# Performance work log

Measured on AMD Instinct MI355X. Metric: run time of the kernel, lower is better.

Reference implementation:

```python
import jax, jax.numpy as jnp
import numpy as np

D = 1024
H = 16
HD = D // H
B = 2
T = 2048


def _rope_tables(t, hd):
    inv_freq = 1.0 / (10000.0 ** (np.arange(0, hd, 2, dtype=np.float32) / hd))
    ang = np.arange(t, dtype=np.float32)[:, None] * inv_freq[None, :]  # [T, hd/2]
    emb = np.concatenate([ang, ang], axis=-1)  # [T, hd]
    return jnp.asarray(np.cos(emb)), jnp.asarray(np.sin(emb))


def setup_inputs() -> dict:
    key = jax.random.key(0)
    kx, kq, kk, kv, ko = jax.random.split(key, 5)
    scale = 0.02
    x = jax.random.normal(kx, (B, T, D), dtype=jnp.float32)
    cos, sin = _rope_tables(T, HD)
    mask = jnp.tril(jnp.ones((T, T), dtype=jnp.int32))[None, None]  # [1,1,T,T]
    wq = jax.random.normal(kq, (D, D), dtype=jnp.float32) * scale
    wk = jax.random.normal(kk, (D, D), dtype=jnp.float32) * scale
    wv = jax.random.normal(kv, (D, D), dtype=jnp.float32) * scale
    wo = jax.random.normal(ko, (D, D), dtype=jnp.float32) * scale
    return {"x": x, "cos": cos, "sin": sin, "mask": mask,
            "wq": wq, "wk": wk, "wv": wv, "wo": wo}


def _rotate_half(t):
    t1, t2 = jnp.split(t, 2, axis=-1)
    return jnp.concatenate((-t2, t1), axis=-1)


def reference(x, cos, sin, mask, wq, wk, wv, wo):
    Bx, Tx, C = x.shape
    hd = C // H
    # nn.Linear: y = x @ W.T  -> [B,T,H,hd] -> [B,H,T,hd]
    q = (x @ wq.T).reshape(Bx, Tx, H, hd).transpose(0, 2, 1, 3)
    k = (x @ wk.T).reshape(Bx, Tx, H, hd).transpose(0, 2, 1, 3)
    v = (x @ wv.T).reshape(Bx, Tx, H, hd).transpose(0, 2, 1, 3)
    c = cos[:Tx][None, None]  # [1,1,T,hd]
    s = sin[:Tx][None, None]
    q = q * c + _rotate_half(q) * s
    k = k * c + _rotate_half(k) * s
    att = jnp.einsum('bhqd,bhkd->bhqk', q, k) * (hd ** -0.5)
    att = jnp.where(mask[:, :, :Tx, :Tx] == 0, -jnp.inf, att)
    att = jax.nn.softmax(att, axis=-1)
    out = jnp.einsum('bhqk,bhkd->bhqd', att, v)
    out = out.transpose(0, 2, 1, 3).reshape(Bx, Tx, C)
    return out @ wo.T
```

## Files before the change

### kernel.cpp

```cpp
#include <hip/hip_runtime.h>
#include <math.h>

constexpr int D  = 1024;
constexpr int H  = 16;
constexpr int HD = 64;
constexpr int B  = 2;
constexpr int T  = 2048;
constexpr int M  = B * T;

constexpr size_t XSZ = (size_t)M * D;
constexpr size_t WSZ = (size_t)D * D;

typedef float  f32x4   __attribute__((ext_vector_type(4)));
typedef float  f32x16  __attribute__((ext_vector_type(16)));
typedef __bf16 bf16x8  __attribute__((ext_vector_type(8)));
typedef __bf16 bf16x4  __attribute__((ext_vector_type(4)));
typedef unsigned u32x2 __attribute__((ext_vector_type(2)));
typedef unsigned u32x4 __attribute__((ext_vector_type(4)));

static __device__ inline f32x4 mfma16(bf16x8 a, bf16x8 b, f32x4 c) {
  return __builtin_amdgcn_mfma_f32_16x16x32_bf16(a, b, c, 0, 0, 0);
}
static __device__ inline f32x16 mfma32(bf16x8 a, bf16x8 b, f32x16 c) {
  return __builtin_amdgcn_mfma_f32_32x32x16_bf16(a, b, c, 0, 0, 0);
}
static __device__ inline unsigned cvtpk(float a, float b) {
  unsigned r;
  asm("v_cvt_pk_bf16_f32 %0, %1, %2" : "=v"(r) : "v"(a), "v"(b));
  return r;
}
static __device__ inline u32x2 plswap(unsigned a, unsigned b) {
  return __builtin_amdgcn_permlane32_swap(a, b, false, false);
}
static __device__ inline void gload16(const __bf16* g, __bf16* l) {
  __builtin_amdgcn_global_load_lds(
      (const __attribute__((address_space(1))) void*)g,
      (__attribute__((address_space(3))) void*)l, 16, 0, 0);
}

__global__ __launch_bounds__(256)
void cvt_all(const float* __restrict__ x, const float* __restrict__ wq,
             const float* __restrict__ wk, const float* __restrict__ wv,
             const float* __restrict__ wo, __bf16* __restrict__ out) {
  size_t idx = ((size_t)blockIdx.x * 256 + threadIdx.x) * 8;
  const float* src;
  if      (idx < XSZ)            src = x  + idx;
  else if (idx < XSZ + WSZ)      src = wq + (idx - XSZ);
  else if (idx < XSZ + 2 * WSZ)  src = wk + (idx - XSZ - WSZ);
  else if (idx < XSZ + 3 * WSZ)  src = wv + (idx - XSZ - 2 * WSZ);
  else                           src = wo + (idx - XSZ - 3 * WSZ);
  float4 a = *reinterpret_cast<const float4*>(src);
  float4 b = *reinterpret_cast<const float4*>(src + 4);
  bf16x8 o;
  o[0] = (__bf16)a.x; o[1] = (__bf16)a.y; o[2] = (__bf16)a.z; o[3] = (__bf16)a.w;
  o[4] = (__bf16)b.x; o[5] = (__bf16)b.y; o[6] = (__bf16)b.z; o[7] = (__bf16)b.w;
  *reinterpret_cast<bf16x8*>(out + idx) = o;
}

template<int MODE>
__global__ __launch_bounds__(256)
void gemm_mfma(const __bf16* __restrict__ A,
               const __bf16* __restrict__ W0, const __bf16* __restrict__ W1,
               const __bf16* __restrict__ W2,
               const float* __restrict__ cosT, const float* __restrict__ sinT,
               void* __restrict__ out0, void* __restrict__ out1,
               void* __restrict__ out2) {
  constexpr int BM  = (MODE == 0) ? 64 : 128;
  constexpr int NMT = BM / 32;
  __shared__ __bf16 As[BM * 64];
  __shared__ __bf16 Bs[128 * 64];

  const int tid  = threadIdx.x;
  const int lane = tid & 63;
  const int w    = tid >> 6;
  const int wm   = w >> 1;
  const int wn   = w & 1;
  const int l15  = lane & 15, lg = lane >> 4;
  const int m0   = blockIdx.y * BM;

  int which, n0;
  const __bf16* Bw;
  if (MODE == 1) {
    which = blockIdx.x >> 3;
    n0 = (blockIdx.x & 7) * 128;
    Bw = which == 0 ? W0 : which == 1 ? W1 : W2;
  } else {
    which = 0;
    n0 = blockIdx.x * 128;
    Bw = W0;
  }

  f32x4 acc[NMT][4];
  #pragma unroll
  for (int i = 0; i < NMT; ++i)
    #pragma unroll
    for (int j = 0; j < 4; ++j) acc[i][j] = (f32x4){0.f, 0.f, 0.f, 0.f};

  const int r0 = tid >> 3;
  const int c0 = (tid & 7) * 8;

  for (int k0 = 0; k0 < 1024; k0 += 64) {
    #pragma unroll
    for (int i = 0; i < BM / 32; ++i)
      gload16(A + (size_t)(m0 + r0 + 32 * i) * 1024 + k0 + c0,
              As + (tid + 256 * i) * 8);
    #pragma unroll
    for (int i = 0; i < 4; ++i)
      gload16(Bw + (size_t)(n0 + r0 + 32 * i) * 1024 + k0 + c0,
              Bs + (tid + 256 * i) * 8);
    __syncthreads();

    #pragma unroll
    for (int ks = 0; ks < 2; ++ks) {
      bf16x8 af[NMT], bfr[4];
      #pragma unroll
      for (int mt = 0; mt < NMT; ++mt)
        af[mt] = *reinterpret_cast<const bf16x8*>(
            &As[(wm * (BM / 2) + mt * 16 + l15) * 64 + ks * 32 + lg * 8]);
      #pragma unroll
      for (int nt = 0; nt < 4; ++nt)
        bfr[nt] = *reinterpret_cast<const bf16x8*>(
            &Bs[(wn * 64 + nt * 16 + l15) * 64 + ks * 32 + lg * 8]);
      #pragma unroll
      for (int mt = 0; mt < NMT; ++mt)
        #pragma unroll
        for (int nt = 0; nt < 4; ++nt)
          acc[mt][nt] = mfma16(af[mt], bfr[nt], acc[mt][nt]);
    }
    __syncthreads();
  }

  if (MODE == 0) {
    float* o = (float*)out0;
    #pragma unroll
    for (int mt = 0; mt < NMT; ++mt) {
      const int mb = m0 + wm * (BM / 2) + mt * 16 + lg * 4;
      #pragma unroll
      for (int nt = 0; nt < 4; ++nt) {
        const int n = n0 + wn * 64 + nt * 16 + l15;
        #pragma unroll
        for (int r = 0; r < 4; ++r)
          o[(size_t)(mb + r) * 1024 + n] = acc[mt][nt][r];
      }
    }
  } else if (which < 2) {
    __bf16* dst = which == 0 ? (__bf16*)out0 : (__bf16*)out1;
    const float qs = (which == 0) ? 0.180336880f : 1.0f;
    const int h = (n0 + wn * 64) >> 6;
    const int e  = l15 & 7;
    const int Lh = (l15 >> 3) << 5;
    #pragma unroll
    for (int mt = 0; mt < NMT; ++mt) {
      const int tb   = m0 + wm * (BM / 2) + mt * 16 + lg * 4;
      const int bb   = tb >> 11;
      const int tloc = tb & 2047;
      const int bh   = bb * H + h;
      #pragma unroll
      for (int r = 0; r < 4; ++r) {
        const int t = tloc + r;
        const int L = (t & 31) + Lh;
        size_t fb;
        if (which == 0)
          fb = ((size_t)bh * 64 + (t >> 5)) * 4;
        else
          fb = (((size_t)bh * 32 + (t >> 6)) * 2 + ((t >> 5) & 1)) * 4;
        #pragma unroll
        for (int nt = 0; nt < 2; ++nt) {
          const int hd = nt * 16 + l15;
          const float c = cosT[t * HD + hd];
          const float s = sinT[t * HD + hd];
          const float v1 = acc[mt][nt][r];
          const float v2 = acc[mt][nt + 2][r];
          dst[(fb + nt)     * 512 + L * 8 + e] = (__bf16)((v1 * c - v2 * s) * qs);
          dst[(fb + nt + 2) * 512 + L * 8 + e] = (__bf16)((v2 * c + v1 * s) * qs);
        }
      }
    }
  } else {
    __bf16* dst = (__bf16*)out2;
    const int h = (n0 + wn * 64) >> 6;
    #pragma unroll
    for (int mt = 0; mt < NMT; ++mt) {
      const int tb   = m0 + wm * (BM / 2) + mt * 16 + lg * 4;
      const int bb   = tb >> 11;
      const int tloc = tb & 2047;
      const int bh   = bb * H + h;
      const int jt   = tloc >> 6;
      const int kt   = tloc & 63;
      const int Lk   = ((kt >> 3) & 1) << 5;
      const int e0   = kt & 7;
      const size_t fb = (((size_t)bh * 32 + jt) * 2) * 4 + (kt >> 4);
      #pragma unroll
      for (int nt = 0; nt < 4; ++nt) {
        const int hd = nt * 16 + l15;
        const int dg = hd >> 5;
        const int L  = (hd & 31) + Lk;
        bf16x4 ov;
        #pragma unroll
        for (int r = 0; r < 4; ++r) ov[r] = (__bf16)acc[mt][nt][r];
        *reinterpret_cast<bf16x4*>(
            &dst[(fb + (size_t)dg * 4) * 512 + L * 8 + e0]) = ov;
      }
    }
  }
}

__global__ __launch_bounds__(256, 2)
void attn_v15(const __bf16* __restrict__ Qf, const __bf16* __restrict__ Kf,
              const __bf16* __restrict__ Vf, __bf16* __restrict__ Ob) {
  const int tid  = threadIdx.x;
  const int lane = tid & 63;
  const int w    = tid >> 6;
  const int l31  = lane & 31;
  const int hi   = lane >> 5;
  const int bx   = blockIdx.x;
  const int by   = blockIdx.y;
  const int bh   = (bx & 7) + 8 * (by >> 3);
  const int x    = (bx >> 3) + 2 * (by & 7);

  const int wi = (bh < 16) ? w : (w ^ 1);
  const int qt = (wi == 0) ? 2 * x : (wi == 1) ? 63 - 2 * x
               : (wi == 2) ? 2 * x + 1 : 62 - 2 * x;
  const int q0w = qt * 32;
  const int NT  = (qt >> 1) + 1;

  const __bf16* qbase = Qf + (((size_t)bh * 64 + qt) * 4) * 512 + lane * 8;
  bf16x8 qfr[4];
  #pragma unroll
  for (int st = 0; st < 4; ++st)
    qfr[st] = *reinterpret_cast<const bf16x8*>(qbase + st * 512);

  f32x16 zv;
  #pragma unroll
  for (int i = 0; i < 16; ++i) zv[i] = 0.f;

  float m_run = -INFINITY, l_run = 0.f;
  f32x16 oacc0, oacc1;
  #pragma unroll
  for (int i = 0; i < 16; ++i) { oacc0[i] = 0.f; oacc1[i] = 0.f; }

  const __bf16* kbase = Kf + ((size_t)bh * 32 * 8) * 512 + lane * 8;
  const __bf16* vbase = Vf + ((size_t)bh * 32 * 8) * 512 + lane * 8;

#define LOADK8(K0, K1, K2, K3, K4, K5, K6, K7, jj)                            \
  do {                                                                        \
    const __bf16* _kp = kbase + (size_t)(jj) * 8 * 512;                       \
    K0 = *reinterpret_cast<const bf16x8*>(_kp);                               \
    K1 = *reinterpret_cast<const bf16x8*>(_kp + 512);                         \
    K2 = *reinterpret_cast<const bf16x8*>(_kp + 1024);                        \
    K3 = *reinterpret_cast<const bf16x8*>(_kp + 1536);                        \
    K4 = *reinterpret_cast<const bf16x8*>(_kp + 2048);                        \
    K5 = *reinterpret_cast<const bf16x8*>(_kp + 2560);                        \
    K6 = *reinterpret_cast<const bf16x8*>(_kp + 3072);                        \
    K7 = *reinterpret_cast<const bf16x8*>(_kp + 3584);                        \
    __builtin_amdgcn_sched_barrier(0);                                        \
  } while (0)

#define LOADV8(jj)                                                            \
  do {                                                                        \
    const __bf16* _vp = vbase + (size_t)(jj) * 8 * 512;                       \
    VV0 = *reinterpret_cast<const bf16x8*>(_vp);                              \
    VV1 = *reinterpret_cast<const bf16x8*>(_vp + 512);                        \
    VV2 = *reinterpret_cast<const bf16x8*>(_vp + 1024);                       \
    VV3 = *reinterpret_cast<const bf16x8*>(_vp + 1536);                       \
    VV4 = *reinterpret_cast<const bf16x8*>(_vp + 2048);                       \
    VV5 = *reinterpret_cast<const bf16x8*>(_vp + 2560);                       \
    VV6 = *reinterpret_cast<const bf16x8*>(_vp + 3072);                       \
    VV7 = *reinterpret_cast<const bf16x8*>(_vp + 3584);                       \
    __builtin_amdgcn_sched_barrier(0);                                        \
  } while (0)

#define QK64(SV0, SV1, K0, K1, K2, K3, K4, K5, K6, K7)                        \
  do {                                                                        \
    SV0 = mfma32(K0, qfr[0], zv);                                             \
    SV0 = mfma32(K1, qfr[1], SV0);                                            \
    SV0 = mfma32(K2, qfr[2], SV0);                                            \
    SV0 = mfma32(K3, qfr[3], SV0);                                            \
    SV1 = mfma32(K4, qfr[0], zv);                                             \
    SV1 = mfma32(K5, qfr[1], SV1);                                            \
    SV1 = mfma32(K6, qfr[2], SV1);                                            \
    SV1 = mfma32(K7, qfr[3], SV1);                                            \
  } while (0)

#define SMPV(SV0, SV1, jj)                                                    \
  do {                                                                        \
    if ((jj) == NT - 1) {         \
      const int _q  = q0w + l31;                                              \
      const int _k0 = (jj) * 64 + 4 * hi;                                     \
      _Pragma("unroll")                                                       \
      for (int _r = 0; _r < 16; ++_r) {                                       \
        const int _key = _k0 + (_r & 3) + 8 * (_r >> 2);                      \
        if (_key > _q)      SV0[_r] = -INFINITY;                              \
        if (_key + 32 > _q) SV1[_r] = -INFINITY;                              \
      }                                                                       \
    }                                                                         \
    float _mx[16];                                                            \
    _Pragma("unroll")                                                         \
    for (int _i = 0; _i < 16; ++_i) _mx[_i] = fmaxf(SV0[_i], SV1[_i]);        \
    _Pragma("unroll")                                                         \
    for (int _s = 8; _s > 0; _s >>= 1)                                        \
      _Pragma("unroll")                                                       \
      for (int _i = 0; _i < 8; ++_i)                                          \
        if (_i < _s) _mx[_i] = fmaxf(_mx[_i], _mx[_i + _s]);                  \
    union { float f; unsigned u; } _cv; _cv.f = _mx[0];                       \
    u32x2 _sw = plswap(_cv.u, _cv.u);                                         \
    union { unsigned u; float f; } _c0, _c1; _c0.u = _sw[0]; _c1.u = _sw[1];  \
    const float _pmax = fmaxf(_c0.f, _c1.f);                                  \
    if (__any(_pmax > m_run + 8.f)) {                                         \
      const float _mn = fmaxf(m_run, _pmax);                                  \
      const float _rs = exp2f(m_run - _mn);                                   \
      l_run *= _rs;                                                           \
      _Pragma("unroll")                                                       \
      for (int _i = 0; _i < 16; ++_i) { oacc0[_i] *= _rs; oacc1[_i] *= _rs; } \
      m_run = _mn;                                                            \
    }                                                                         \
    _Pragma("unroll")                                                         \
    for (int _i = 0; _i < 16; ++_i) {                                         \
      SV0[_i] = exp2f(SV0[_i] - m_run);                                       \
      SV1[_i] = exp2f(SV1[_i] - m_run);                                       \
    }                                                                         \
    float _sm[16];                                                            \
    _Pragma("unroll")                                                         \
    for (int _i = 0; _i < 16; ++_i) _sm[_i] = SV0[_i] + SV1[_i];              \
    _Pragma("unroll")                                                         \
    for (int _s = 8; _s > 0; _s >>= 1)                                        \
      _Pragma("unroll")                                                       \
      for (int _i = 0; _i < 8; ++_i)                                          \
        if (_i < _s) _sm[_i] += _sm[_i + _s];                                 \
    l_run += _sm[0];                                                          \
    unsigned _cp0[8], _cp1[8];                                                \
    _Pragma("unroll")                                                         \
    for (int _m = 0; _m < 4; ++_m) {                                          \
      _cp0[2 * _m]     = cvtpk(SV0[4 * _m],     SV0[4 * _m + 1]);             \
      _cp0[2 * _m + 1] = cvtpk(SV0[4 * _m + 2], SV0[4 * _m + 3]);             \
      _cp1[2 * _m]     = cvtpk(SV1[4 * _m],     SV1[4 * _m + 1]);             \
      _cp1[2 * _m + 1] = cvtpk(SV1[4 * _m + 2], SV1[4 * _m + 3]);             \
    }                                                                         \
    {                                                                         \
      u32x2 _r0 = plswap(_cp0[0], _cp0[2]);                                   \
      u32x2 _r1 = plswap(_cp0[1], _cp0[3]);                                   \
      union { u32x4 u; bf16x8 v; } _pu;                                       \
      _pu.u = (u32x4){_r0[0], _r1[0], _r0[1], _r1[1]};                        \
      oacc0 = mfma32(VV0, _pu.v, oacc0);                                      \
      oacc1 = mfma32(VV4, _pu.v, oacc1);                                      \
    }                                                                         \
    {                                                                         \
      u32x2 _r0 = plswap(_cp0[4], _cp0[6]);                                   \
      u32x2 _r1 = plswap(_cp0[5], _cp0[7]);                                   \
      union { u32x4 u; bf16x8 v; } _pu;                                       \
      _pu.u = (u32x4){_r0[0], _r1[0], _r0[1], _r1[1]};                        \
      oacc0 = mfma32(VV1, _pu.v, oacc0);                                      \
      oacc1 = mfma32(VV5, _pu.v, oacc1);                                      \
    }                                                                         \
    {                                                                         \
      u32x2 _r0 = plswap(_cp1[0], _cp1[2]);                                   \
      u32x2 _r1 = plswap(_cp1[1], _cp1[3]);                                   \
      union { u32x4 u; bf16x8 v; } _pu;                                       \
      _pu.u = (u32x4){_r0[0], _r1[0], _r0[1], _r1[1]};                        \
      oacc0 = mfma32(VV2, _pu.v, oacc0);                                      \
      oacc1 = mfma32(VV6, _pu.v, oacc1);                                      \
    }                                                                         \
    {                                                                         \
      u32x2 _r0 = plswap(_cp1[4], _cp1[6]);                                   \
      u32x2 _r1 = plswap(_cp1[5], _cp1[7]);                                   \
      union { u32x4 u; bf16x8 v; } _pu;                                       \
      _pu.u = (u32x4){_r0[0], _r1[0], _r0[1], _r1[1]};                        \
      oacc0 = mfma32(VV3, _pu.v, oacc0);                                      \
      oacc1 = mfma32(VV7, _pu.v, oacc1);                                      \
    }                                                                         \
  } while (0)

  bf16x8 kA0, kA1, kA2, kA3, kA4, kA5, kA6, kA7;
  bf16x8 kB0, kB1, kB2, kB3, kB4, kB5, kB6, kB7;
  bf16x8 VV0, VV1, VV2, VV3, VV4, VV5, VV6, VV7;
  f32x16 svA0, svA1, svB0, svB1;

  LOADK8(kA0, kA1, kA2, kA3, kA4, kA5, kA6, kA7, 0);
  QK64(svA0, svA1, kA0, kA1, kA2, kA3, kA4, kA5, kA6, kA7);
  if (1 < NT) LOADK8(kB0, kB1, kB2, kB3, kB4, kB5, kB6, kB7, 1);

  int j = 0;
  #pragma unroll 1
  for (;;) {
    LOADV8(j);
    if (j + 1 < NT)
      QK64(svB0, svB1, kB0, kB1, kB2, kB3, kB4, kB5, kB6, kB7);
    if (j + 2 < NT)
      LOADK8(kA0, kA1, kA2, kA3, kA4, kA5, kA6, kA7, j + 2);
    SMPV(svA0, svA1, j);
    if (++j >= NT) break;

    LOADV8(j);
    if (j + 1 < NT)
      QK64(svA0, svA1, kA0, kA1, kA2, kA3, kA4, kA5, kA6, kA7);
    if (j + 2 < NT)
      LOADK8(kB0, kB1, kB2, kB3, kB4, kB5, kB6, kB7, j + 2);
    SMPV(svB0, svB1, j);
    if (++j >= NT) break;
  }
#undef SMPV
#undef QK64
#undef LOADV8
#undef LOADK8

  const float l_tot = l_run + __shfl_xor(l_run, 32);
  const float inv = 1.f / l_tot;
  const int b = bh >> 4, h = bh & 15;
  const int q_abs = q0w + l31;
  const size_t rowbase = ((size_t)(b * T + q_abs)) * 1024 + h * 64;
  #pragma unroll
  for (int rg = 0; rg < 4; ++rg) {
    bf16x4 o0, o1;
    #pragma unroll
    for (int r = 0; r < 4; ++r) {
      o0[r] = (__bf16)(oacc0[rg * 4 + r] * inv);
      o1[r] = (__bf16)(oacc1[rg * 4 + r] * inv);
    }
    *reinterpret_cast<bf16x4*>(&Ob[rowbase + rg * 8 + hi * 4])      = o0;
    *reinterpret_cast<bf16x4*>(&Ob[rowbase + 32 + rg * 8 + hi * 4]) = o1;
  }
}

extern "C" void kernel_launch(void* const* d_in, const int* in_sizes, int n_in,
                              void* d_out, int out_size, void* d_ws, size_t ws_size,
                              hipStream_t stream) {
  const float* x    = (const float*)d_in[0];
  const float* cosT = (const float*)d_in[1];
  const float* sinT = (const float*)d_in[2];
  const float* wq   = (const float*)d_in[4];
  const float* wk   = (const float*)d_in[5];
  const float* wv   = (const float*)d_in[6];
  const float* wo   = (const float*)d_in[7];
  float* out = (float*)d_out;

  __bf16* xb   = (__bf16*)d_ws;
  __bf16* wqb  = xb  + XSZ;
  __bf16* wkb  = wqb + WSZ;
  __bf16* wvb  = wkb + WSZ;
  __bf16* wob  = wvb + WSZ;
  __bf16* Qfb  = wob + WSZ;
  __bf16* Kfb  = Qfb + XSZ;
  __bf16* Vfb  = Kfb + XSZ;
  __bf16* attb = Vfb + XSZ;

  cvt_all<<<(XSZ + 4 * WSZ) / 8 / 256, 256, 0, stream>>>(x, wq, wk, wv, wo, xb);

  gemm_mfma<1><<<dim3(24, 32), 256, 0, stream>>>(
      xb, wqb, wkb, wvb, cosT, sinT, Qfb, Kfb, Vfb);

  attn_v15<<<dim3(16, 32), 256, 0, stream>>>(Qfb, Kfb, Vfb, attb);

  gemm_mfma<0><<<dim3(8, 64), 256, 0, stream>>>(
      attb, wob, nullptr, nullptr, nullptr, nullptr, out, nullptr, nullptr);
}
```

Before: 141.3 us.

## Share A tile across Q, K and V weights in fused QKV GEMM

The QKV projection kernel now has each block load one 64-row activation tile and all three weight tiles, computing the Q, K and V outputs together. Previously blocks were split by weight matrix with a 128-row A tile, so each activation tile was fetched three times. This trades A reuse for more shared memory (about 56KB) and three times the accumulator registers per thread, which may cut occupancy. The output projection is split into its own non-templated kernel with the same tiling as before.

```diff
diff --git a/kernel.cpp b/kernel.cpp
--- a/kernel.cpp
+++ b/kernel.cpp
@@ -57,18 +57,15 @@
   *reinterpret_cast<bf16x8*>(out + idx) = o;
 }
 
-template<int MODE>
 __global__ __launch_bounds__(256)
-void gemm_mfma(const __bf16* __restrict__ A,
-               const __bf16* __restrict__ W0, const __bf16* __restrict__ W1,
-               const __bf16* __restrict__ W2,
-               const float* __restrict__ cosT, const float* __restrict__ sinT,
-               void* __restrict__ out0, void* __restrict__ out1,
-               void* __restrict__ out2) {
-  constexpr int BM  = (MODE == 0) ? 64 : 128;
-  constexpr int NMT = BM / 32;
-  __shared__ __bf16 As[BM * 64];
-  __shared__ __bf16 Bs[128 * 64];
+void gemm_qkv(const __bf16* __restrict__ A,
+              const __bf16* __restrict__ W0, const __bf16* __restrict__ W1,
+              const __bf16* __restrict__ W2,
+              const float* __restrict__ cosT, const float* __restrict__ sinT,
+              __bf16* __restrict__ Qf, __bf16* __restrict__ Kf,
+              __bf16* __restrict__ Vf) {
+  __shared__ __bf16 As[64 * 64];
+  __shared__ __bf16 Bs[3][128 * 64];
 
   const int tid  = threadIdx.x;
   const int lane = tid & 63;
@@ -76,112 +73,98 @@
   const int wm   = w >> 1;
   const int wn   = w & 1;
   const int l15  = lane & 15, lg = lane >> 4;
-  const int m0   = blockIdx.y * BM;
-
-  int which, n0;
-  const __bf16* Bw;
-  if (MODE == 1) {
-    which = blockIdx.x >> 3;
-    n0 = (blockIdx.x & 7) * 128;
-    Bw = which == 0 ? W0 : which == 1 ? W1 : W2;
-  } else {
-    which = 0;
-    n0 = blockIdx.x * 128;
-    Bw = W0;
-  }
-
-  f32x4 acc[NMT][4];
-  #pragma unroll
-  for (int i = 0; i < NMT; ++i)
-    #pragma unroll
-    for (int j = 0; j < 4; ++j) acc[i][j] = (f32x4){0.f, 0.f, 0.f, 0.f};
+  const int m0   = blockIdx.y * 64;
+  const int n0   = blockIdx.x * 128;
+
+  f32x4 acc[3][2][4];
+  #pragma unroll
+  for (int ws = 0; ws < 3; ++ws)
+    #pragma unroll
+    for (int i = 0; i < 2; ++i)
+      #pragma unroll
+      for (int j = 0; j < 4; ++j) acc[ws][i][j] = (f32x4){0.f, 0.f, 0.f, 0.f};
 
   const int r0 = tid >> 3;
   const int c0 = (tid & 7) * 8;
 
   for (int k0 = 0; k0 < 1024; k0 += 64) {
-    #pragma unroll
-    for (int i = 0; i < BM / 32; ++i)
-      gload16(A + (size_t)(m0 + r0 + 32 * i) * 1024 + k0 + c0,
-              As + (tid + 256 * i) * 8);
-    #pragma unroll
-    for (int i = 0; i < 4; ++i)
-      gload16(Bw + (size_t)(n0 + r0 + 32 * i) * 1024 + k0 + c0,
-              Bs + (tid + 256 * i) * 8);
+    gload16(A + (size_t)(m0 + r0) * 1024 + k0 + c0,      As + tid * 8);
+    gload16(A + (size_t)(m0 + r0 + 32) * 1024 + k0 + c0, As + (tid + 256) * 8);
+    #pragma unroll
+    for (int i = 0; i < 4; ++i) {
+      const size_t go = (size_t)(n0 + r0 + 32 * i) * 1024 + k0 + c0;
+      gload16(W0 + go, Bs[0] + (tid + 256 * i) * 8);
+      gload16(W1 + go, Bs[1] + (tid + 256 * i) * 8);
+      gload16(W2 + go, Bs[2] + (tid + 256 * i) * 8);
+    }
     __syncthreads();
 
     #pragma unroll
     for (int ks = 0; ks < 2; ++ks) {
-      bf16x8 af[NMT], bfr[4];
-      #pragma unroll
-      for (int mt = 0; mt < NMT; ++mt)
+      bf16x8 af[2];
+      #pragma unroll
+      for (int mt = 0; mt < 2; ++mt)
         af[mt] = *reinterpret_cast<const bf16x8*>(
-            &As[(wm * (BM / 2) + mt * 16 + l15) * 64 + ks * 32 + lg * 8]);
-      #pragma unroll
-      for (int nt = 0; nt < 4; ++nt)
-        bfr[nt] = *reinterpret_cast<const bf16x8*>(
-            &Bs[(wn * 64 + nt * 16 + l15) * 64 + ks * 32 + lg * 8]);
-      #pragma unroll
-      for (int mt = 0; mt < NMT; ++mt)
+            &As[(wm * 32 + mt * 16 + l15) * 64 + ks * 32 + lg * 8]);
+      #pragma unroll
+      for (int ws = 0; ws < 3; ++ws) {
+        bf16x8 bfr[4];
         #pragma unroll
         for (int nt = 0; nt < 4; ++nt)
-          acc[mt][nt] = mfma16(af[mt], bfr[nt], acc[mt][nt]);
+          bfr[nt] = *reinterpret_cast<const bf16x8*>(
+              &Bs[ws][(wn * 64 + nt * 16 + l15) * 64 + ks * 32 + lg * 8]);
+        #pragma unroll
+        for (int mt = 0; mt < 2; ++mt)
+          #pragma unroll
+          for (int nt = 0; nt < 4; ++nt)
+            acc[ws][mt][nt] = mfma16(af[mt], bfr[nt], acc[ws][mt][nt]);
+      }
     }
     __syncthreads();
   }
 
-  if (MODE == 0) {
-    float* o = (float*)out0;
-    #pragma unroll
-    for (int mt = 0; mt < NMT; ++mt) {
-      const int mb = m0 + wm * (BM / 2) + mt * 16 + lg * 4;
-      #pragma unroll
-      for (int nt = 0; nt < 4; ++nt) {
-        const int n = n0 + wn * 64 + nt * 16 + l15;
-        #pragma unroll
-        for (int r = 0; r < 4; ++r)
-          o[(size_t)(mb + r) * 1024 + n] = acc[mt][nt][r];
-      }
-    }
-  } else if (which < 2) {
-    __bf16* dst = which == 0 ? (__bf16*)out0 : (__bf16*)out1;
-    const float qs = (which == 0) ? 0.180336880f : 1.0f;
-    const int h = (n0 + wn * 64) >> 6;
+  {
+    const int h  = (n0 + wn * 64) >> 6;
     const int e  = l15 & 7;
     const int Lh = (l15 >> 3) << 5;
     #pragma unroll
-    for (int mt = 0; mt < NMT; ++mt) {
-      const int tb   = m0 + wm * (BM / 2) + mt * 16 + lg * 4;
-      const int bb   = tb >> 11;
-      const int tloc = tb & 2047;
-      const int bh   = bb * H + h;
-      #pragma unroll
-      for (int r = 0; r < 4; ++r) {
-        const int t = tloc + r;
-        const int L = (t & 31) + Lh;
-        size_t fb;
-        if (which == 0)
-          fb = ((size_t)bh * 64 + (t >> 5)) * 4;
-        else
-          fb = (((size_t)bh * 32 + (t >> 6)) * 2 + ((t >> 5) & 1)) * 4;
+    for (int ws = 0; ws < 2; ++ws) {
+      __bf16* dst = (ws == 0) ? Qf : Kf;
+      const float qs = (ws == 0) ? 0.180336880f : 1.0f;
+      #pragma unroll
+      for (int mt = 0; mt < 2; ++mt) {
+        const int tb   = m0 + wm * 32 + mt * 16 + lg * 4;
+        const int bb   = tb >> 11;
+        const int tloc = tb & 2047;
+        const int bh   = bb * H + h;
         #pragma unroll
-        for (int nt = 0; nt < 2; ++nt) {
-          const int hd = nt * 16 + l15;
-          const float c = cosT[t * HD + hd];
-          const float s = sinT[t * HD + hd];
-          const float v1 = acc[mt][nt][r];
-          const float v2 = acc[mt][nt + 2][r];
-          dst[(fb + nt)     * 512 + L * 8 + e] = (__bf16)((v1 * c - v2 * s) * qs);
-          dst[(fb + nt + 2) * 512 + L * 8 + e] = (__bf16)((v2 * c + v1 * s) * qs);
+        for (int r = 0; r < 4; ++r) {
+          const int t = tloc + r;
+          const int L = (t & 31) + Lh;
+          size_t fb;
+          if (ws == 0)
+            fb = ((size_t)bh * 64 + (t >> 5)) * 4;
+          else
+            fb = (((size_t)bh * 32 + (t >> 6)) * 2 + ((t >> 5) & 1)) * 4;
+          #pragma unroll
+          for (int nt = 0; nt < 2; ++nt) {
+            const int hd = nt * 16 + l15;
+            const float c = cosT[t * HD + hd];
+            const float s = sinT[t * HD + hd];
+            const float v1 = acc[ws][mt][nt][r];
+            const float v2 = acc[ws][mt][nt + 2][r];
+            dst[(fb + nt)     * 512 + L * 8 + e] = (__bf16)((v1 * c - v2 * s) * qs);
+            dst[(fb + nt + 2) * 512 + L * 8 + e] = (__bf16)((v2 * c + v1 * s) * qs);
+          }
         }
       }
     }
-  } else {
-    __bf16* dst = (__bf16*)out2;
+  }
+  {
     const int h = (n0 + wn * 64) >> 6;
     #pragma unroll
-    for (int mt = 0; mt < NMT; ++mt) {
-      const int tb   = m0 + wm * (BM / 2) + mt * 16 + lg * 4;
+    for (int mt = 0; mt < 2; ++mt) {
+      const int tb   = m0 + wm * 32 + mt * 16 + lg * 4;
       const int bb   = tb >> 11;
       const int tloc = tb & 2047;
       const int bh   = bb * H + h;
@@ -197,10 +180,76 @@
         const int L  = (hd & 31) + Lk;
         bf16x4 ov;
         #pragma unroll
-        for (int r = 0; r < 4; ++r) ov[r] = (__bf16)acc[mt][nt][r];
+        for (int r = 0; r < 4; ++r) ov[r] = (__bf16)acc[2][mt][nt][r];
         *reinterpret_cast<bf16x4*>(
-            &dst[(fb + (size_t)dg * 4) * 512 + L * 8 + e0]) = ov;
+            &Vf[(fb + (size_t)dg * 4) * 512 + L * 8 + e0]) = ov;
       }
+    }
+  }
+}
+
+__global__ __launch_bounds__(256)
+void gemm_wo(const __bf16* __restrict__ A, const __bf16* __restrict__ W0,
+             float* __restrict__ out) {
+  __shared__ __bf16 As[64 * 64];
+  __shared__ __bf16 Bs[128 * 64];
+
+  const int tid  = threadIdx.x;
+  const int lane = tid & 63;
+  const int w    = tid >> 6;
+  const int wm   = w >> 1;
+  const int wn   = w & 1;
+  const int l15  = lane & 15, lg = lane >> 4;
+  const int m0   = blockIdx.y * 64;
+  const int n0   = blockIdx.x * 128;
+
+  f32x4 acc[2][4];
+  #pragma unroll
+  for (int i = 0; i < 2; ++i)
+    #pragma unroll
+    for (int j = 0; j < 4; ++j) acc[i][j] = (f32x4){0.f, 0.f, 0.f, 0.f};
+
+  const int r0 = tid >> 3;
+  const int c0 = (tid & 7) * 8;
+
+  for (int k0 = 0; k0 < 1024; k0 += 64) {
+    gload16(A + (size_t)(m0 + r0) * 1024 + k0 + c0,      As + tid * 8);
+    gload16(A + (size_t)(m0 + r0 + 32) * 1024 + k0 + c0, As + (tid + 256) * 8);
+    #pragma unroll
+    for (int i = 0; i < 4; ++i)
+      gload16(W0 + (size_t)(n0 + r0 + 32 * i) * 1024 + k0 + c0,
+              Bs + (tid + 256 * i) * 8);
+    __syncthreads();
+
+    #pragma unroll
+    for (int ks = 0; ks < 2; ++ks) {
+      bf16x8 af[2], bfr[4];
+      #pragma unroll
+      for (int mt = 0; mt < 2; ++mt)
+        af[mt] = *reinterpret_cast<const bf16x8*>(
+            &As[(wm * 32 + mt * 16 + l15) * 64 + ks * 32 + lg * 8]);
+      #pragma unroll
+      for (int nt = 0; nt < 4; ++nt)
+        bfr[nt] = *reinterpret_cast<const bf16x8*>(
+            &Bs[(wn * 64 + nt * 16 + l15) * 64 + ks * 32 + lg * 8]);
+      #pragma unroll
+      for (int mt = 0; mt < 2; ++mt)
+        #pragma unroll
+        for (int nt = 0; nt < 4; ++nt)
+          acc[mt][nt] = mfma16(af[mt], bfr[nt], acc[mt][nt]);
+    }
+    __syncthreads();
+  }
+
+  #pragma unroll
+  for (int mt = 0; mt < 2; ++mt) {
+    const int mb = m0 + wm * 32 + mt * 16 + lg * 4;
+    #pragma unroll
+    for (int nt = 0; nt < 4; ++nt) {
+      const int n = n0 + wn * 64 + nt * 16 + l15;
+      #pragma unroll
+      for (int r = 0; r < 4; ++r)
+        out[(size_t)(mb + r) * 1024 + n] = acc[mt][nt][r];
     }
   }
 }
@@ -284,7 +333,7 @@
 
 #define SMPV(SV0, SV1, jj)                                                    \
   do {                                                                        \
-    if ((jj) == NT - 1) {         \
+    if ((jj) == NT - 1) {                                                     \
       const int _q  = q0w + l31;                                              \
       const int _k0 = (jj) * 64 + 4 * hi;                                     \
       _Pragma("unroll")                                                       \
@@ -445,11 +494,10 @@
 
   cvt_all<<<(XSZ + 4 * WSZ) / 8 / 256, 256, 0, stream>>>(x, wq, wk, wv, wo, xb);
 
-  gemm_mfma<1><<<dim3(24, 32), 256, 0, stream>>>(
+  gemm_qkv<<<dim3(8, 64), 256, 0, stream>>>(
       xb, wqb, wkb, wvb, cosT, sinT, Qfb, Kfb, Vfb);
 
   attn_v15<<<dim3(16, 32), 256, 0, stream>>>(Qfb, Kfb, Vfb, attb);
 
-  gemm_mfma<0><<<dim3(8, 64), 256, 0, stream>>>(
-      attb, wob, nullptr, nullptr, nullptr, nullptr, out, nullptr, nullptr);
-}
+  gemm_wo<<<dim3(8, 64), 256, 0, stream>>>(attb, wob, out);
+}
```

Result: slower. 160.5 us (+13.6%).

## Software-pipeline attention K/V loads with inline asm and explicit vmcnt waits

Applied to the files above, without the earlier changes.

Replaces compiler-generated K/V global loads with inline-asm global_load_dwordx4 instructions and manual s_waitcnt vmcnt counters. The loop is restructured so the V tile for the next step is issued right after softmax, and K loads run two tiles ahead with clamped indices instead of conditional branches. This lets loads stay in flight across the QK and softmax/PV work, and it drops one pair of score accumulators, which frees registers. The cost is redundant loads on the final iterations and fragile manual wait counts, which could read stale data if the counts are wrong.

```diff
diff --git a/kernel.cpp b/kernel.cpp
--- a/kernel.cpp
+++ b/kernel.cpp
@@ -205,8 +205,17 @@
   }
 }
 
+#define GLDO(dst, ptr, OFF)                                                   \
+  asm volatile("global_load_dwordx4 %0, %1, off offset:" #OFF                 \
+               : "=&v"(dst) : "v"(ptr) : "memory")
+#define WAITN(N)                                                              \
+  do {                                                                        \
+    asm volatile("s_waitcnt vmcnt(" #N ")" ::: "memory");                     \
+    __builtin_amdgcn_sched_barrier(0);                                        \
+  } while (0)
+
 __global__ __launch_bounds__(256, 2)
-void attn_v15(const __bf16* __restrict__ Qf, const __bf16* __restrict__ Kf,
+void attn_v18(const __bf16* __restrict__ Qf, const __bf16* __restrict__ Kf,
               const __bf16* __restrict__ Vf, __bf16* __restrict__ Ob) {
   const int tid  = threadIdx.x;
   const int lane = tid & 63;
@@ -244,59 +253,51 @@
 
 #define LOADK8(K0, K1, K2, K3, K4, K5, K6, K7, jj)                            \
   do {                                                                        \
-    const __bf16* _kp = kbase + (size_t)(jj) * 8 * 512;                       \
-    K0 = *reinterpret_cast<const bf16x8*>(_kp);                               \
-    K1 = *reinterpret_cast<const bf16x8*>(_kp + 512);                         \
-    K2 = *reinterpret_cast<const bf16x8*>(_kp + 1024);                        \
-    K3 = *reinterpret_cast<const bf16x8*>(_kp + 1536);                        \
-    K4 = *reinterpret_cast<const bf16x8*>(_kp + 2048);                        \
-    K5 = *reinterpret_cast<const bf16x8*>(_kp + 2560);                        \
-    K6 = *reinterpret_cast<const bf16x8*>(_kp + 3072);                        \
-    K7 = *reinterpret_cast<const bf16x8*>(_kp + 3584);                        \
-    __builtin_amdgcn_sched_barrier(0);                                        \
+    const __bf16* _p0 = kbase + (size_t)(jj) * 4096;                          \
+    const __bf16* _p1 = _p0 + 2048;                                           \
+    GLDO(K0, _p0, 0);    GLDO(K1, _p0, 1024);                                 \
+    GLDO(K2, _p0, 2048); GLDO(K3, _p0, 3072);                                 \
+    GLDO(K4, _p1, 0);    GLDO(K5, _p1, 1024);                                 \
+    GLDO(K6, _p1, 2048); GLDO(K7, _p1, 3072);                                 \
   } while (0)
 
 #define LOADV8(jj)                                                            \
   do {                                                                        \
-    const __bf16* _vp = vbase + (size_t)(jj) * 8 * 512;                       \
-    VV0 = *reinterpret_cast<const bf16x8*>(_vp);                              \
-    VV1 = *reinterpret_cast<const bf16x8*>(_vp + 512);                        \
-    VV2 = *reinterpret_cast<const bf16x8*>(_vp + 1024);                       \
-    VV3 = *reinterpret_cast<const bf16x8*>(_vp + 1536);                       \
-    VV4 = *reinterpret_cast<const bf16x8*>(_vp + 2048);                       \
-    VV5 = *reinterpret_cast<const bf16x8*>(_vp + 2560);                       \
-    VV6 = *reinterpret_cast<const bf16x8*>(_vp + 3072);                       \
-    VV7 = *reinterpret_cast<const bf16x8*>(_vp + 3584);                       \
-    __builtin_amdgcn_sched_barrier(0);                                        \
+    const __bf16* _p0 = vbase + (size_t)(jj) * 4096;                          \
+    const __bf16* _p1 = _p0 + 2048;                                           \
+    GLDO(VV0, _p0, 0);    GLDO(VV1, _p0, 1024);                               \
+    GLDO(VV2, _p0, 2048); GLDO(VV3, _p0, 3072);                               \
+    GLDO(VV4, _p1, 0);    GLDO(VV5, _p1, 1024);                               \
+    GLDO(VV6, _p1, 2048); GLDO(VV7, _p1, 3072);                               \
   } while (0)
 
-#define QK64(SV0, SV1, K0, K1, K2, K3, K4, K5, K6, K7)                        \
+#define QK64(K0, K1, K2, K3, K4, K5, K6, K7)                                  \
   do {                                                                        \
-    SV0 = mfma32(K0, qfr[0], zv);                                             \
-    SV0 = mfma32(K1, qfr[1], SV0);                                            \
-    SV0 = mfma32(K2, qfr[2], SV0);                                            \
-    SV0 = mfma32(K3, qfr[3], SV0);                                            \
-    SV1 = mfma32(K4, qfr[0], zv);                                             \
-    SV1 = mfma32(K5, qfr[1], SV1);                                            \
-    SV1 = mfma32(K6, qfr[2], SV1);                                            \
-    SV1 = mfma32(K7, qfr[3], SV1);                                            \
+    sv0 = mfma32(K0, qfr[0], zv);                                             \
+    sv0 = mfma32(K1, qfr[1], sv0);                                            \
+    sv0 = mfma32(K2, qfr[2], sv0);                                            \
+    sv0 = mfma32(K3, qfr[3], sv0);                                            \
+    sv1 = mfma32(K4, qfr[0], zv);                                             \
+    sv1 = mfma32(K5, qfr[1], sv1);                                            \
+    sv1 = mfma32(K6, qfr[2], sv1);                                            \
+    sv1 = mfma32(K7, qfr[3], sv1);                                            \
   } while (0)
 
-#define SMPV(SV0, SV1, jj)                                                    \
+#define SMPV(jj)                                                              \
   do {                                                                        \
-    if ((jj) == NT - 1) {         \
+    if ((jj) == NT - 1) {                          \
       const int _q  = q0w + l31;                                              \
       const int _k0 = (jj) * 64 + 4 * hi;                                     \
       _Pragma("unroll")                                                       \
       for (int _r = 0; _r < 16; ++_r) {                                       \
         const int _key = _k0 + (_r & 3) + 8 * (_r >> 2);                      \
-        if (_key > _q)      SV0[_r] = -INFINITY;                              \
-        if (_key + 32 > _q) SV1[_r] = -INFINITY;                              \
+        if (_key > _q)      sv0[_r] = -INFINITY;                              \
+        if (_key + 32 > _q) sv1[_r] = -INFINITY;                              \
       }                                                                       \
     }                                                                         \
     float _mx[16];                                                            \
     _Pragma("unroll")                                                         \
-    for (int _i = 0; _i < 16; ++_i) _mx[_i] = fmaxf(SV0[_i], SV1[_i]);        \
+    for (int _i = 0; _i < 16; ++_i) _mx[_i] = fmaxf(sv0[_i], sv1[_i]);        \
     _Pragma("unroll")                                                         \
     for (int _s = 8; _s > 0; _s >>= 1)                                        \
       _Pragma("unroll")                                                       \
@@ -316,12 +317,12 @@
     }                                                                         \
     _Pragma("unroll")                                                         \
     for (int _i = 0; _i < 16; ++_i) {                                         \
-      SV0[_i] = exp2f(SV0[_i] - m_run);                                       \
-      SV1[_i] = exp2f(SV1[_i] - m_run);                                       \
+      sv0[_i] = exp2f(sv0[_i] - m_run);                                       \
+      sv1[_i] = exp2f(sv1[_i] - m_run);                                       \
     }                                                                         \
     float _sm[16];                                                            \
     _Pragma("unroll")                                                         \
-    for (int _i = 0; _i < 16; ++_i) _sm[_i] = SV0[_i] + SV1[_i];              \
+    for (int _i = 0; _i < 16; ++_i) _sm[_i] = sv0[_i] + sv1[_i];              \
     _Pragma("unroll")                                                         \
     for (int _s = 8; _s > 0; _s >>= 1)                                        \
       _Pragma("unroll")                                                       \
@@ -331,10 +332,10 @@
     unsigned _cp0[8], _cp1[8];                                                \
     _Pragma("unroll")                                                         \
     for (int _m = 0; _m < 4; ++_m) {                                          \
-      _cp0[2 * _m]     = cvtpk(SV0[4 * _m],     SV0[4 * _m + 1]);             \
-      _cp0[2 * _m + 1] = cvtpk(SV0[4 * _m + 2], SV0[4 * _m + 3]);             \
-      _cp1[2 * _m]     = cvtpk(SV1[4 * _m],     SV1[4 * _m + 1]);             \
-      _cp1[2 * _m + 1] = cvtpk(SV1[4 * _m + 2], SV1[4 * _m + 3]);             \
+      _cp0[2 * _m]     = cvtpk(sv0[4 * _m],     sv0[4 * _m + 1]);             \
+      _cp0[2 * _m + 1] = cvtpk(sv0[4 * _m + 2], sv0[4 * _m + 3]);             \
+      _cp1[2 * _m]     = cvtpk(sv1[4 * _m],     sv1[4 * _m + 1]);             \
+      _cp1[2 * _m + 1] = cvtpk(sv1[4 * _m + 2], sv1[4 * _m + 3]);             \
     }                                                                         \
     {                                                                         \
       u32x2 _r0 = plswap(_cp0[0], _cp0[2]);                                   \
@@ -373,31 +374,41 @@
   bf16x8 kA0, kA1, kA2, kA3, kA4, kA5, kA6, kA7;
   bf16x8 kB0, kB1, kB2, kB3, kB4, kB5, kB6, kB7;
   bf16x8 VV0, VV1, VV2, VV3, VV4, VV5, VV6, VV7;
-  f32x16 svA0, svA1, svB0, svB1;
+  f32x16 sv0, sv1;
 
   LOADK8(kA0, kA1, kA2, kA3, kA4, kA5, kA6, kA7, 0);
-  QK64(svA0, svA1, kA0, kA1, kA2, kA3, kA4, kA5, kA6, kA7);
-  if (1 < NT) LOADK8(kB0, kB1, kB2, kB3, kB4, kB5, kB6, kB7, 1);
+  {
+    const int j1 = (1 < NT) ? 1 : 0;
+    LOADK8(kB0, kB1, kB2, kB3, kB4, kB5, kB6, kB7, j1);
+  }
+  LOADV8(0);
+  WAITN(16);
 
   int j = 0;
   #pragma unroll 1
   for (;;) {
+    QK64(kA0, kA1, kA2, kA3, kA4, kA5, kA6, kA7);
+    {
+      const int jn = (j + 2 < NT) ? j + 2 : NT - 1;
+      LOADK8(kA0, kA1, kA2, kA3, kA4, kA5, kA6, kA7, jn);
+    }
+    WAITN(8);
+    SMPV(j);
+    if (++j >= NT) break;
     LOADV8(j);
-    if (j + 1 < NT)
-      QK64(svB0, svB1, kB0, kB1, kB2, kB3, kB4, kB5, kB6, kB7);
-    if (j + 2 < NT)
-      LOADK8(kA0, kA1, kA2, kA3, kA4, kA5, kA6, kA7, j + 2);
-    SMPV(svA0, svA1, j);
+
+    QK64(kB0, kB1, kB2, kB3, kB4, kB5, kB6, kB7);
+    {
+      const int jn = (j + 2 < NT) ? j + 2 : NT - 1;
+      LOADK8(kB0, kB1, kB2, kB3, kB4, kB5, kB6, kB7, jn);
+    }
+    WAITN(8);
+    SMPV(j);
     if (++j >= NT) break;
-
     LOADV8(j);
-    if (j + 1 < NT)
-      QK64(svA0, svA1, kA0, kA1, kA2, kA3, kA4, kA5, kA6, kA7);
-    if (j + 2 < NT)
-      LOADK8(kB0, kB1, kB2, kB3, kB4, kB5, kB6, kB7, j + 2);
-    SMPV(svB0, svB1, j);
-    if (++j >= NT) break;
-  }
+  }
+  asm volatile("s_waitcnt vmcnt(0)" ::: "memory");
+  __builtin_amdgcn_sched_barrier(0);
 #undef SMPV
 #undef QK64
 #undef LOADV8
@@ -448,7 +459,7 @@
   gemm_mfma<1><<<dim3(24, 32), 256, 0, stream>>>(
       xb, wqb, wkb, wvb, cosT, sinT, Qfb, Kfb, Vfb);
 
-  attn_v15<<<dim3(16, 32), 256, 0, stream>>>(Qfb, Kfb, Vfb, attb);
+  attn_v18<<<dim3(16, 32), 256, 0, stream>>>(Qfb, Kfb, Vfb, attb);
 
   gemm_mfma<0><<<dim3(8, 64), 256, 0, stream>>>(
       attb, wob, nullptr, nullptr, nullptr, nullptr, out, nullptr, nullptr);
```

Result: slower. 144.8 us (+2.5%).
